# Kernel tuning notes

Measured on AMD Instinct MI355X. Metric: run time of the kernel, lower is better.

## Reference

```python
import math
import jax, jax.numpy as jnp
import numpy as np
from jax import lax

DN = ('NCHW', 'OIHW', 'NCHW')

def _blur(x):
    # upfirdn2d blur: separable [1,3,3,1] kernel, normalized, gain=factor^2=4, pad (1,1)
    k1 = jnp.asarray([1., 3., 3., 1.], dtype=x.dtype)
    k2 = jnp.outer(k1, k1)
    k2 = k2 / jnp.sum(k2) * 4.0
    C = x.shape[1]
    kern = jnp.broadcast_to(k2[None, None], (C, 1, 4, 4))
    return lax.conv_general_dilated(x, kern, (1, 1), [(1, 1), (1, 1)],
                                    feature_group_count=C, dimension_numbers=DN)

def _mod_conv(x, z, w, mw, mb, demodulate, upsample):
    # StyleGAN2 ModulatedConv2d. w: [Co,Ci,k,k]; mw: [Ci,style_dim]; mb: [Ci].
    # Equivalent formulation: scale input by style (per in-channel), conv with
    # base weight, rescale output by per-sample demod (per out-channel).
    Ci, k = w.shape[1], w.shape[-1]
    style = z @ mw.T * (1.0 / math.sqrt(mw.shape[1])) + mb  # EqualLinear -> [B, Ci]
    ws = w * (1.0 / math.sqrt(Ci * k * k))
    if demodulate:
        wmod = ws[None] * style[:, None, :, None, None]              # [B,Co,Ci,k,k]
        demod = lax.rsqrt(jnp.sum(wmod * wmod, axis=(2, 3, 4)) + 1e-8)  # [B,Co]
    x = x * style[:, :, None, None]
    if upsample:
        # torch conv_transpose2d(stride=2, pad=0) == direct conv with flipped kernel + lhs dilation
        kern = ws[:, :, ::-1, ::-1]
        x = lax.conv_general_dilated(x, kern, (1, 1), [(k - 1, k - 1)] * 2,
                                     lhs_dilation=(2, 2), dimension_numbers=DN)
    else:
        x = lax.conv_general_dilated(x, ws, (1, 1), [(k // 2, k // 2)] * 2,
                                     dimension_numbers=DN)
    if demodulate:
        x = x * demod[:, :, None, None]
    if upsample:
        x = _blur(x)
    return x

def _styled_conv(x, z, w, mw, mb, b, upsample):
    # StyledConv (use_noise=False): modulated conv + FusedLeakyReLU(bias, 0.2, gain sqrt(2))
    x = _mod_conv(x, z, w, mw, mb, True, upsample)
    return jax.nn.leaky_relu(x + b[None, :, None, None], 0.2) * math.sqrt(2.0)

def setup_inputs() -> dict:
    B, CIN, SD, S = 16, 256, 512, 32
    key = jax.random.key(0)
    ks = jax.random.split(key, 32)
    f32 = jnp.float32
    d = {
        'fg_feat': jax.random.normal(ks[0], (B, CIN, S, S), f32),
        'mask':    jax.random.uniform(ks[1], (B, S, S), f32),
        'bg_feat': jax.random.normal(ks[2], (B, CIN, S, S), f32),
        'z':       jax.random.normal(ks[3], (B, SD), f32),
    }
    # layer schedule: (cin, cout, upsample)
    layers = [(CIN, 128, False), (128, 128, True), (128, 64, False),
              (64, 64, True), (64, 32, False)]
    i = 4
    for li, (ci, co, _) in enumerate(layers):
        d[f'l{li}_w'] = jax.random.normal(ks[i], (co, ci, 3, 3), f32); i += 1
        d[f'l{li}_mw'] = jax.random.normal(ks[i], (ci, SD), f32); i += 1
        d[f'l{li}_mb'] = jnp.ones((ci,), f32)
        d[f'l{li}_b'] = jnp.zeros((co,), f32)
    d['fin_w'] = jax.random.normal(ks[i], (4, 32, 1, 1), f32); i += 1
    d['fin_mw'] = jax.random.normal(ks[i], (32, SD), f32); i += 1
    d['fin_mb'] = jnp.ones((32,), f32)
    d['out_bias'] = jnp.zeros((1, 4, 1, 1), f32)
    return d

def reference(fg_feat, mask, bg_feat, z,
              l0_w, l0_mw, l0_mb, l0_b,
              l1_w, l1_mw, l1_mb, l1_b,
              l2_w, l2_mw, l2_mb, l2_b,
              l3_w, l3_mw, l3_mb, l3_b,
              l4_w, l4_mw, l4_mb, l4_b,
              fin_w, fin_mw, fin_mb, out_bias):
    # bg_activation is None -> no bg transform
    h = fg_feat + (1.0 - mask[:, None]) * bg_feat          # [B,256,32,32]
    h = _styled_conv(h, z, l0_w, l0_mw, l0_mb, l0_b, False)  # [B,128,32,32]
    h = _styled_conv(h, z, l1_w, l1_mw, l1_mb, l1_b, True)   # [B,128,64,64]
    h = _styled_conv(h, z, l2_w, l2_mw, l2_mb, l2_b, False)  # [B,64,64,64]
    h = _styled_conv(h, z, l3_w, l3_mw, l3_mb, l3_b, True)   # [B,64,128,128]
    h = _styled_conv(h, z, l4_w, l4_mw, l4_mb, l4_b, False)  # [B,32,128,128]
    h = _mod_conv(h, z, fin_w, fin_mw, fin_mb, False, False) + out_bias  # [B,4,128,128]
    return h[:, :3]
```

## Files before the change

kernel.cpp:

```cpp
#include <hip/hip_runtime.h>
#include <math.h>

#define SQRT2 1.41421356237309515f

typedef __bf16 bf16x8 __attribute__((ext_vector_type(8)));
typedef float f32x4 __attribute__((ext_vector_type(4)));
typedef unsigned short u16x4 __attribute__((ext_vector_type(4)));
typedef unsigned short u16x8 __attribute__((ext_vector_type(8)));

__device__ __forceinline__ unsigned short f2bf(float f) {
    unsigned u = __builtin_bit_cast(unsigned, f);
    u += 0x7fffu + ((u >> 16) & 1u);
    return (unsigned short)(u >> 16);
}

__global__ __launch_bounds__(256) void style_all(
    const float* __restrict__ z,
    const float* __restrict__ mw0, const float* __restrict__ mb0,
    const float* __restrict__ mw1, const float* __restrict__ mb1,
    const float* __restrict__ mw2, const float* __restrict__ mb2,
    const float* __restrict__ mw3, const float* __restrict__ mb3,
    const float* __restrict__ mw4, const float* __restrict__ mb4,
    const float* __restrict__ mwf, const float* __restrict__ mbf,
    float* __restrict__ s0, float* __restrict__ s1, float* __restrict__ s2,
    float* __restrict__ s3, float* __restrict__ s4, float* __restrict__ sf) {
    int i = blockIdx.x * 256 + threadIdx.x;
    const float* mw; const float* mb; float* o; int Ci, idx; float mul = 1.f;
    if (i < 4096)       { mw = mw0; mb = mb0; o = s0; Ci = 256; idx = i; }
    else if (i < 6144)  { mw = mw1; mb = mb1; o = s1; Ci = 128; idx = i - 4096; }
    else if (i < 8192)  { mw = mw2; mb = mb2; o = s2; Ci = 128; idx = i - 6144; }
    else if (i < 9216)  { mw = mw3; mb = mb3; o = s3; Ci = 64;  idx = i - 8192; }
    else if (i < 10240) { mw = mw4; mb = mb4; o = s4; Ci = 64;  idx = i - 9216; }
    else if (i < 10752) { mw = mwf; mb = mbf; o = sf; Ci = 32;  idx = i - 10240;
                          mul = 0.1767766952966369f; }
    else return;
    int b = idx / Ci, ci = idx % Ci;
    const float* zp = z + b * 512;
    const float* wp = mw + ci * 512;
    float acc = 0.f;
#pragma unroll 8
    for (int k = 0; k < 512; ++k) acc += zp[k] * wp[k];
    o[idx] = (acc * 0.04419417382415922f + mb[ci]) * mul;
}

__global__ __launch_bounds__(256) void demod_all(
    const float* __restrict__ w0, const float* __restrict__ w1,
    const float* __restrict__ w2, const float* __restrict__ w3,
    const float* __restrict__ w4,
    const float* __restrict__ s0, const float* __restrict__ s1,
    const float* __restrict__ s2, const float* __restrict__ s3,
    const float* __restrict__ s4,
    float* __restrict__ d0, float* __restrict__ d1, float* __restrict__ d2,
    float* __restrict__ d3, float* __restrict__ d4) {
    int wid = blockIdx.x * 4 + (threadIdx.x >> 6);
    int lane = threadIdx.x & 63;
    const float* w; const float* s; float* d; int Co, Ci, idx;
    if (wid < 2048)      { w = w0; s = s0; d = d0; Co = 128; Ci = 256; idx = wid; }
    else if (wid < 4096) { w = w1; s = s1; d = d1; Co = 128; Ci = 128; idx = wid - 2048; }
    else if (wid < 5120) { w = w2; s = s2; d = d2; Co = 64;  Ci = 128; idx = wid - 4096; }
    else if (wid < 6144) { w = w3; s = s3; d = d3; Co = 64;  Ci = 64;  idx = wid - 5120; }
    else if (wid < 6656) { w = w4; s = s4; d = d4; Co = 32;  Ci = 64;  idx = wid - 6144; }
    else return;
    int b = idx / Co, co = idx % Co;
    const float* wp = w + (size_t)co * Ci * 9;
    const float* sp = s + b * Ci;
    float acc = 0.f;
    for (int k = lane; k < Ci * 9; k += 64) {
        int ci = k / 9;
        float v = wp[k], sv = sp[ci];
        acc += v * v * sv * sv;
    }
    for (int off = 32; off > 0; off >>= 1) acc += __shfl_down(acc, off);
    if (lane == 0) d[b * Co + co] = rsqrtf(acc / (float)(Ci * 9) + 1e-8f);
}

__device__ __forceinline__ void pack_cw_elem(
    const float* __restrict__ w, unsigned short* __restrict__ dst,
    int i, int Ci, int KT, float sInv) {
    int cil = i & 31;
    int r = i >> 5;
    int col = r % 32; r /= 32;
    int t = r % 9; r /= 9;
    int c = r % KT, g = r / KT;
    int co = g * 32 + col, ci = c * 32 + cil;
    dst[i] = f2bf(w[((size_t)co * Ci + ci) * 9 + t] * sInv);
}
__device__ __forceinline__ void pack_fused_elem(
    const float* __restrict__ w, unsigned short* __restrict__ dst,
    int i, int Ci, int KT, float sInv) {
    int cil = i & 31;
    int r = i >> 5;
    int col = r % 32; r /= 32;
    int t = r % 36; r /= 36;
    int c = r % KT, g = r / KT;
    int co = g * 32 + col, ci = c * 32 + cil;
    int p = t / 9, dd = (t % 9) / 3, ee = t % 3;
    int py = p >> 1, px = p & 1;
    const float k1[4] = {1.f, 3.f, 3.f, 1.f};
    const float* wq = w + ((size_t)co * Ci + ci) * 9;
    float acc = 0.f;
#pragma unroll
    for (int rr = 0; rr < 3; ++rr) {
        int ia = 2 * dd + rr - 1 - py;
        if (ia < 0 || ia > 3) continue;
#pragma unroll
        for (int ss = 0; ss < 3; ++ss) {
            int ib = 2 * ee + ss - 1 - px;
            if (ib < 0 || ib > 3) continue;
            acc += wq[rr * 3 + ss] * k1[ia] * k1[ib];
        }
    }
    dst[i] = f2bf(acc * sInv * (1.f / 16.f));
}

__global__ __launch_bounds__(256) void pack_all(
    const float* __restrict__ l0w, const float* __restrict__ l1w,
    const float* __restrict__ l2w, const float* __restrict__ l3w,
    const float* __restrict__ l4w, unsigned short* __restrict__ base) {
    const float sInv1152 = 0.02946278254943948f;
    int i = blockIdx.x * 256 + threadIdx.x;
    if (i < 294912)       pack_cw_elem(l0w, base, i, 256, 8, 1.f / 48.f);
    else if (i < 368640)  pack_cw_elem(l2w, base + 294912, i - 294912, 128, 4, sInv1152);
    else if (i < 387072)  pack_cw_elem(l4w, base + 368640, i - 368640, 64, 2, 1.f / 24.f);
    else if (i < 976896)  pack_fused_elem(l1w, base + 387072, i - 387072, 128, 4, sInv1152);
    else if (i < 1124352) pack_fused_elem(l3w, base + 976896, i - 976896, 64, 2, 1.f / 24.f);
}

__global__ __launch_bounds__(256) void composite_cl_kernel(
    const float* __restrict__ fg, const float* __restrict__ mask,
    const float* __restrict__ bg, const float* __restrict__ sty0,
    unsigned short* __restrict__ out) {
    __shared__ unsigned short ldsT[32 * 264];
    int blk = blockIdx.x;
    int b = blk >> 5, y = blk & 31;
    int t = threadIdx.x;
    int x = t & 31, cr = t >> 5;
    const float* sb = sty0 + b * 256;
    float m = 1.f - mask[(b << 10) + (y << 5) + x];
    for (int k = 0; k < 32; ++k) {
        int ci = k * 8 + cr;
        size_t idx = ((size_t)(b * 256 + ci) << 10) + (y << 5) + x;
        float v = fg[idx] + m * bg[idx];
        ldsT[x * 264 + ci] = f2bf(v * sb[ci]);
    }
    __syncthreads();
    int xx = t >> 5, cu = t & 31;
#pragma unroll
    for (int ph = 0; ph < 4; ++ph) {
        int px = ph * 8 + xx;
        u16x8 v = *(const u16x8*)&ldsT[px * 264 + cu * 8];
        *(u16x8*)(out + (((size_t)(b * 32 + y) * 32 + px) << 8) + cu * 8) = v;
    }
}

template <int OUTMODE>
__global__ __launch_bounds__(256, 4) void conv3x3_cl(
    const unsigned short* __restrict__ X, const unsigned short* __restrict__ W,
    const float* __restrict__ demod, const float* __restrict__ bias,
    const float* __restrict__ nextsty, const float* __restrict__ finw,
    const float* __restrict__ ob, void* __restrict__ outv,
    int Ci, int Co, int S, int TPS, int KCH, int cogN) {
    __shared__ unsigned short ldsX[324 * 40];
    const int tid = threadIdx.x;
    const int b = blockIdx.z;
    const int gy_ = blockIdx.y;
    const int ks = gy_ / cogN, cog = gy_ % cogN;
    const int tile = blockIdx.x;
    const int ty0 = (tile / TPS) * 16, tx0 = (tile % TPS) * 16;
    const int KT = Ci >> 5;
    const int wave = tid >> 6, lane = tid & 63, quad = lane >> 4, l16 = lane & 15;

    f32x4 acc[2][4];
#pragma unroll
    for (int mt = 0; mt < 2; ++mt)
#pragma unroll
        for (int nt = 0; nt < 4; ++nt) acc[mt][nt] = (f32x4){0.f, 0.f, 0.f, 0.f};

    for (int cc = 0; cc < KCH; ++cc) {
        const int cg = ks * KCH + cc;
        const int ci0 = cg * 32;
        for (int u = tid; u < 1296; u += 256) {
            int sp = u >> 2, cq = u & 3;
            int y = sp / 18, xx = sp - y * 18;
            int gy = ty0 - 1 + y, gx = tx0 - 1 + xx;
            u16x8 pk = (u16x8){0, 0, 0, 0, 0, 0, 0, 0};
            if ((unsigned)gy < (unsigned)S && (unsigned)gx < (unsigned)S)
                pk = *(const u16x8*)(X + ((size_t)(b * S + gy) * S + gx) * Ci + ci0 + cq * 8);
            *(u16x8*)&ldsX[sp * 40 + cq * 8] = pk;
        }
        __syncthreads();
        const unsigned short* wt = W + (((size_t)cog * KT + cg) * 9) * 1024;
#pragma unroll
        for (int t = 0; t < 9; ++t) {
            const int ty = t / 3, tx = t - ty * 3;
            bf16x8 af[2];
#pragma unroll
            for (int mt = 0; mt < 2; ++mt)
                af[mt] = *(const bf16x8*)(const void*)(wt + t * 1024 + (mt * 16 + l16) * 32 + quad * 8);
#pragma unroll
            for (int nt = 0; nt < 4; ++nt) {
                int sp = (wave * 4 + nt + ty) * 18 + l16 + tx;
                bf16x8 bv = *(const bf16x8*)(const void*)&ldsX[sp * 40 + quad * 8];
#pragma unroll
                for (int mt = 0; mt < 2; ++mt)
                    acc[mt][nt] = __builtin_amdgcn_mfma_f32_16x16x32_bf16(af[mt], bv, acc[mt][nt], 0, 0, 0);
            }
        }
        __syncthreads();
    }
    const int col = tx0 + l16;
    if (OUTMODE == 0) {
        float* out = (float*)outv;
        const size_t PS = (size_t)16 * S * S * Co;
#pragma unroll
        for (int mt = 0; mt < 2; ++mt) {
            int co0 = cog * 32 + mt * 16 + quad * 4;
#pragma unroll
            for (int nt = 0; nt < 4; ++nt) {
                int row = ty0 + wave * 4 + nt;
                *(f32x4*)&out[ks * PS + ((size_t)(b * S + row) * S + col) * Co + co0] = acc[mt][nt];
            }
        }
    } else if (OUTMODE == 1) {
#pragma unroll
        for (int mt = 0; mt < 2; ++mt) {
            int co0 = cog * 32 + mt * 16 + quad * 4;
            f32x4 dm = *(const f32x4*)&demod[b * Co + co0];
            f32x4 bi = *(const f32x4*)&bias[co0];
            f32x4 ns = *(const f32x4*)&nextsty[b * Co + co0];
#pragma unroll
            for (int nt = 0; nt < 4; ++nt) {
                int row = ty0 + wave * 4 + nt;
                size_t base = ((size_t)(b * S + row) * S + col) * Co + co0;
                u16x4 st;
#pragma unroll
                for (int r = 0; r < 4; ++r) {
                    float v = acc[mt][nt][r] * dm[r] + bi[r];
                    v = (v > 0.f ? v : 0.2f * v) * SQRT2 * ns[r];
                    st[r] = f2bf(v);
                }
                *(u16x4*)((unsigned short*)outv + base) = st;
            }
        }
    } else {
        f32x4 dm[2], bi[2], ns[2];
        float fw[3][2][4];
#pragma unroll
        for (int mt = 0; mt < 2; ++mt) {
            int c0 = mt * 16 + quad * 4;
            dm[mt] = *(const f32x4*)&demod[b * Co + c0];
            bi[mt] = *(const f32x4*)&bias[c0];
            ns[mt] = *(const f32x4*)&nextsty[b * Co + c0];
#pragma unroll
            for (int c = 0; c < 3; ++c)
#pragma unroll
                for (int r = 0; r < 4; ++r) fw[c][mt][r] = finw[c * 32 + c0 + r];
        }
        float* out = (float*)outv;
        float ob0 = ob[0], ob1 = ob[1], ob2 = ob[2];
#pragma unroll
        for (int nt = 0; nt < 4; ++nt) {
            int row = ty0 + wave * 4 + nt;
            float p0 = 0.f, p1 = 0.f, p2 = 0.f;
#pragma unroll
            for (int mt = 0; mt < 2; ++mt)
#pragma unroll
                for (int r = 0; r < 4; ++r) {
                    float v = acc[mt][nt][r] * dm[mt][r] + bi[mt][r];
                    v = (v > 0.f ? v : 0.2f * v) * SQRT2 * ns[mt][r];
                    p0 += v * fw[0][mt][r];
                    p1 += v * fw[1][mt][r];
                    p2 += v * fw[2][mt][r];
                }
            p0 += __shfl_xor(p0, 16); p0 += __shfl_xor(p0, 32);
            p1 += __shfl_xor(p1, 16); p1 += __shfl_xor(p1, 32);
            p2 += __shfl_xor(p2, 16); p2 += __shfl_xor(p2, 32);
            if (quad == 0) {
                size_t base = (((size_t)b * 3) << 14) + (row << 7) + col;
                out[base] = p0 + ob0;
                out[base + 16384] = p1 + ob1;
                out[base + 32768] = p2 + ob2;
            }
        }
    }
}

__global__ __launch_bounds__(256) void combine_l0_kernel(
    const float* __restrict__ P, const float* __restrict__ demod,
    const float* __restrict__ bias, const float* __restrict__ sty1,
    unsigned short* __restrict__ out) {
    int i = blockIdx.x * 256 + threadIdx.x;
    int co = i & 127;
    int b = i >> 17;
    float v = P[i] + P[i + (1 << 21)];
    v = v * demod[b * 128 + co] + bias[co];
    v = (v > 0.f ? v : 0.2f * v) * SQRT2 * sty1[b * 128 + co];
    out[i] = f2bf(v);
}

__global__ __launch_bounds__(256, 4) void upblur_cl(
    const unsigned short* __restrict__ X, const unsigned short* __restrict__ EW,
    const float* __restrict__ demod, const float* __restrict__ bias,
    const float* __restrict__ nextsty, unsigned short* __restrict__ out,
    int Ci, int Co, int S, int TPS) {
    __shared__ unsigned short ldsX[324 * 40];
    const int tid = threadIdx.x;
    const int b = blockIdx.z;
    const int cog = blockIdx.y >> 2, p = blockIdx.y & 3;
    const int tile = blockIdx.x;
    const int ty0 = (tile / TPS) * 16, tx0 = (tile % TPS) * 16;
    const int KT = Ci >> 5;
    const int wave = tid >> 6, lane = tid & 63, quad = lane >> 4, l16 = lane & 15;

    f32x4 acc[2][4];
#pragma unroll
    for (int mt = 0; mt < 2; ++mt)
#pragma unroll
        for (int nt = 0; nt < 4; ++nt) acc[mt][nt] = (f32x4){0.f, 0.f, 0.f, 0.f};

    for (int cc = 0; cc < KT; ++cc) {
        const int ci0 = cc * 32;
        for (int u = tid; u < 1296; u += 256) {
            int sp = u >> 2, cq = u & 3;
            int y = sp / 18, xx = sp - y * 18;
            int gy = ty0 - 1 + y, gx = tx0 - 1 + xx;
            u16x8 pk = (u16x8){0, 0, 0, 0, 0, 0, 0, 0};
            if ((unsigned)gy < (unsigned)S && (unsigned)gx < (unsigned)S)
                pk = *(const u16x8*)(X + ((size_t)(b * S + gy) * S + gx) * Ci + ci0 + cq * 8);
            *(u16x8*)&ldsX[sp * 40 + cq * 8] = pk;
        }
        __syncthreads();
        const unsigned short* wt = EW + (((size_t)cog * KT + cc) * 36 + p * 9) * 1024;
#pragma unroll
        for (int t = 0; t < 9; ++t) {
            const int dd = t / 3, ee = t - dd * 3;
            bf16x8 af[2];
#pragma unroll
            for (int mt = 0; mt < 2; ++mt)
                af[mt] = *(const bf16x8*)(const void*)(wt + t * 1024 + (mt * 16 + l16) * 32 + quad * 8);
#pragma unroll
            for (int nt = 0; nt < 4; ++nt) {
                int sp = (wave * 4 + nt + dd) * 18 + l16 + ee;
                bf16x8 bv = *(const bf16x8*)(const void*)&ldsX[sp * 40 + quad * 8];
#pragma unroll
                for (int mt = 0; mt < 2; ++mt)
                    acc[mt][nt] = __builtin_amdgcn_mfma_f32_16x16x32_bf16(af[mt], bv, acc[mt][nt], 0, 0, 0);
            }
        }
        __syncthreads();
    }
    const int S2 = 2 * S;
    const int py = p >> 1, px = p & 1;
    const int Xc = tx0 + l16, ox = 2 * Xc + px;
#pragma unroll
    for (int mt = 0; mt < 2; ++mt) {
        const int co0 = cog * 32 + mt * 16 + quad * 4;
        f32x4 dm = *(const f32x4*)&demod[b * Co + co0];
        f32x4 bi = *(const f32x4*)&bias[co0];
        f32x4 ns = *(const f32x4*)&nextsty[b * Co + co0];
#pragma unroll
        for (int nt = 0; nt < 4; ++nt) {
            int Y = ty0 + wave * 4 + nt, oy = 2 * Y + py;
            u16x4 st;
#pragma unroll
            for (int r = 0; r < 4; ++r) {
                float v = acc[mt][nt][r] * dm[r] + bi[r];
                v = (v > 0.f ? v : 0.2f * v) * SQRT2 * ns[r];
                st[r] = f2bf(v);
            }
            *(u16x4*)(out + ((size_t)(b * S2 + oy) * S2 + ox) * Co + co0) = st;
        }
    }
}

extern "C" void kernel_launch(void* const* d_in, const int* in_sizes, int n_in,
                              void* d_out, int out_size, void* d_ws, size_t ws_size,
                              hipStream_t stream) {
    const float* fg   = (const float*)d_in[0];
    const float* mask = (const float*)d_in[1];
    const float* bg   = (const float*)d_in[2];
    const float* z    = (const float*)d_in[3];
    const float* l0_w = (const float*)d_in[4];
    const float* l0_mw= (const float*)d_in[5];
    const float* l0_mb= (const float*)d_in[6];
    const float* l0_b = (const float*)d_in[7];
    const float* l1_w = (const float*)d_in[8];
    const float* l1_mw= (const float*)d_in[9];
    const float* l1_mb= (const float*)d_in[10];
    const float* l1_b = (const float*)d_in[11];
    const float* l2_w = (const float*)d_in[12];
    const float* l2_mw= (const float*)d_in[13];
    const float* l2_mb= (const float*)d_in[14];
    const float* l2_b = (const float*)d_in[15];
    const float* l3_w = (const float*)d_in[16];
    const float* l3_mw= (const float*)d_in[17];
    const float* l3_mb= (const float*)d_in[18];
    const float* l3_b = (const float*)d_in[19];
    const float* l4_w = (const float*)d_in[20];
    const float* l4_mw= (const float*)d_in[21];
    const float* l4_mb= (const float*)d_in[22];
    const float* l4_b = (const float*)d_in[23];
    const float* fin_w = (const float*)d_in[24];
    const float* fin_mw= (const float*)d_in[25];
    const float* fin_mb= (const float*)d_in[26];
    const float* obias = (const float*)d_in[27];

    float* wsf = (float*)d_ws;
    float* sty0 = wsf + 0;
    float* sty1 = wsf + 4096;
    float* sty2 = wsf + 6144;
    float* sty3 = wsf + 8192;
    float* sty4 = wsf + 9216;
    float* styf = wsf + 10240;
    float* dm0  = wsf + 10752;
    float* dm1  = wsf + 12800;
    float* dm2  = wsf + 14848;
    float* dm3  = wsf + 15872;
    float* dm4  = wsf + 16896;
    unsigned short* wbase = (unsigned short*)(wsf + 17408);
    unsigned short* wp0 = wbase;
    unsigned short* wp2 = wbase + 294912;
    unsigned short* wp4 = wbase + 368640;
    unsigned short* ew1 = wbase + 387072;
    unsigned short* ew3 = wbase + 976896;
    unsigned short* X0  = (unsigned short*)(wsf + 600000);
    float* Pbuf = wsf + 2697152;
    unsigned short* Y0  = (unsigned short*)(wsf + 6891456);
    unsigned short* Z1  = (unsigned short*)(wsf + 7940032);
    unsigned short* Y2  = X0;
    unsigned short* Z3  = (unsigned short*)(wsf + 12134336);

    dim3 blk(256);

    style_all<<<42, blk, 0, stream>>>(z, l0_mw, l0_mb, l1_mw, l1_mb, l2_mw, l2_mb,
                                      l3_mw, l3_mb, l4_mw, l4_mb, fin_mw, fin_mb,
                                      sty0, sty1, sty2, sty3, sty4, styf);
    demod_all<<<1664, blk, 0, stream>>>(l0_w, l1_w, l2_w, l3_w, l4_w,
                                        sty0, sty1, sty2, sty3, sty4,
                                        dm0, dm1, dm2, dm3, dm4);
    pack_all<<<4392, blk, 0, stream>>>(l0_w, l1_w, l2_w, l3_w, l4_w, wbase);

    composite_cl_kernel<<<512, blk, 0, stream>>>(fg, mask, bg, sty0, X0);

    conv3x3_cl<0><<<dim3(4, 8, 16), blk, 0, stream>>>(X0, wp0, nullptr, nullptr, nullptr, nullptr, nullptr, Pbuf, 256, 128, 32, 2, 4, 4);
    combine_l0_kernel<<<8192, blk, 0, stream>>>(Pbuf, dm0, l0_b, sty1, Y0);

    upblur_cl<<<dim3(4, 16, 16), blk, 0, stream>>>(Y0, ew1, dm1, l1_b, sty2, Z1, 128, 128, 32, 2);

    conv3x3_cl<1><<<dim3(16, 2, 16), blk, 0, stream>>>(Z1, wp2, dm2, l2_b, sty3, nullptr, nullptr, Y2, 128, 64, 64, 4, 4, 2);

    upblur_cl<<<dim3(16, 8, 16), blk, 0, stream>>>(Y2, ew3, dm3, l3_b, sty4, Z3, 64, 64, 64, 4);

    conv3x3_cl<3><<<dim3(64, 1, 16), blk, 0, stream>>>(Z3, wp4, dm4, l4_b, styf, fin_w, obias, (float*)d_out, 64, 32, 128, 8, 2, 1);
}
```

Measured before the change: 303.8 us.

## Drop LDS staging in 3x3 conv kernels; load input fragments directly from global

Both conv3x3_cl and upblur_cl stop staging an 18x18x32 input halo tile in shared memory behind barriers. Each lane now loads its own 6-row column of B fragments straight from global memory, once per horizontal tap, and reuses them across the three vertical taps. This removes the LDS writes and reads and both __syncthreads per channel chunk. In exchange, halo data is fetched redundantly by overlapping waves and lanes, global loads are no longer coalesced through a cooperative loop, and launch bounds drop to 3 blocks per CU to allow more registers.

```diff
diff --git a/kernel.cpp b/kernel.cpp
--- a/kernel.cpp
+++ b/kernel.cpp
@@ -154,17 +154,15 @@
 }
 
 template <int OUTMODE>
-__global__ __launch_bounds__(256, 4) void conv3x3_cl(
+__global__ __launch_bounds__(256, 3) void conv3x3_cl(
     const unsigned short* __restrict__ X, const unsigned short* __restrict__ W,
     const float* __restrict__ demod, const float* __restrict__ bias,
     const float* __restrict__ nextsty, const float* __restrict__ finw,
     const float* __restrict__ ob, void* __restrict__ outv,
     int Ci, int Co, int S, int TPS, int KCH, int cogN) {
-    __shared__ unsigned short ldsX[324 * 40];
     const int tid = threadIdx.x;
     const int b = blockIdx.z;
-    const int gy_ = blockIdx.y;
-    const int ks = gy_ / cogN, cog = gy_ % cogN;
+    const int ks = blockIdx.y / cogN, cog = blockIdx.y % cogN;
     const int tile = blockIdx.x;
     const int ty0 = (tile / TPS) * 16, tx0 = (tile % TPS) * 16;
     const int KT = Ci >> 5;
@@ -176,37 +174,38 @@
 #pragma unroll
         for (int nt = 0; nt < 4; ++nt) acc[mt][nt] = (f32x4){0.f, 0.f, 0.f, 0.f};
 
+    const int gyb = ty0 - 1 + wave * 4;
+    const int gxb = tx0 - 1 + l16;
+
     for (int cc = 0; cc < KCH; ++cc) {
         const int cg = ks * KCH + cc;
-        const int ci0 = cg * 32;
-        for (int u = tid; u < 1296; u += 256) {
-            int sp = u >> 2, cq = u & 3;
-            int y = sp / 18, xx = sp - y * 18;
-            int gy = ty0 - 1 + y, gx = tx0 - 1 + xx;
-            u16x8 pk = (u16x8){0, 0, 0, 0, 0, 0, 0, 0};
-            if ((unsigned)gy < (unsigned)S && (unsigned)gx < (unsigned)S)
-                pk = *(const u16x8*)(X + ((size_t)(b * S + gy) * S + gx) * Ci + ci0 + cq * 8);
-            *(u16x8*)&ldsX[sp * 40 + cq * 8] = pk;
-        }
-        __syncthreads();
-        const unsigned short* wt = W + (((size_t)cog * KT + cg) * 9) * 1024;
-#pragma unroll
-        for (int t = 0; t < 9; ++t) {
-            const int ty = t / 3, tx = t - ty * 3;
-            bf16x8 af[2];
-#pragma unroll
-            for (int mt = 0; mt < 2; ++mt)
-                af[mt] = *(const bf16x8*)(const void*)(wt + t * 1024 + (mt * 16 + l16) * 32 + quad * 8);
-#pragma unroll
-            for (int nt = 0; nt < 4; ++nt) {
-                int sp = (wave * 4 + nt + ty) * 18 + l16 + tx;
-                bf16x8 bv = *(const bf16x8*)(const void*)&ldsX[sp * 40 + quad * 8];
-#pragma unroll
-                for (int mt = 0; mt < 2; ++mt)
-                    acc[mt][nt] = __builtin_amdgcn_mfma_f32_16x16x32_bf16(af[mt], bv, acc[mt][nt], 0, 0, 0);
-            }
-        }
-        __syncthreads();
+        const unsigned short* xb = X + (size_t)cg * 32 + quad * 8;
+        const unsigned short* wt = W + (((size_t)cog * KT + cg) * 9) * 1024 + l16 * 32 + quad * 8;
+#pragma unroll
+        for (int ee = 0; ee < 3; ++ee) {
+            const int gx = gxb + ee;
+            const bool okx = (unsigned)gx < (unsigned)S;
+            bf16x8 bfr[6];
+#pragma unroll
+            for (int rr = 0; rr < 6; ++rr) {
+                int gy = gyb + rr;
+                u16x8 v = (u16x8){0, 0, 0, 0, 0, 0, 0, 0};
+                if (okx && (unsigned)gy < (unsigned)S)
+                    v = *(const u16x8*)(xb + ((size_t)(b * S + gy) * S + gx) * Ci);
+                bfr[rr] = __builtin_bit_cast(bf16x8, v);
+            }
+#pragma unroll
+            for (int ty = 0; ty < 3; ++ty) {
+                const int t = ty * 3 + ee;
+                bf16x8 af0 = *(const bf16x8*)(const void*)(wt + t * 1024);
+                bf16x8 af1 = *(const bf16x8*)(const void*)(wt + t * 1024 + 512);
+#pragma unroll
+                for (int nt = 0; nt < 4; ++nt) {
+                    acc[0][nt] = __builtin_amdgcn_mfma_f32_16x16x32_bf16(af0, bfr[nt + ty], acc[0][nt], 0, 0, 0);
+                    acc[1][nt] = __builtin_amdgcn_mfma_f32_16x16x32_bf16(af1, bfr[nt + ty], acc[1][nt], 0, 0, 0);
+                }
+            }
+        }
     }
     const int col = tx0 + l16;
     if (OUTMODE == 0) {
@@ -298,12 +297,11 @@
     out[i] = f2bf(v);
 }
 
-__global__ __launch_bounds__(256, 4) void upblur_cl(
+__global__ __launch_bounds__(256, 3) void upblur_cl(
     const unsigned short* __restrict__ X, const unsigned short* __restrict__ EW,
     const float* __restrict__ demod, const float* __restrict__ bias,
     const float* __restrict__ nextsty, unsigned short* __restrict__ out,
     int Ci, int Co, int S, int TPS) {
-    __shared__ unsigned short ldsX[324 * 40];
     const int tid = threadIdx.x;
     const int b = blockIdx.z;
     const int cog = blockIdx.y >> 2, p = blockIdx.y & 3;
@@ -318,36 +316,37 @@
 #pragma unroll
         for (int nt = 0; nt < 4; ++nt) acc[mt][nt] = (f32x4){0.f, 0.f, 0.f, 0.f};
 
+    const int gyb = ty0 - 1 + wave * 4;
+    const int gxb = tx0 - 1 + l16;
+
     for (int cc = 0; cc < KT; ++cc) {
-        const int ci0 = cc * 32;
-        for (int u = tid; u < 1296; u += 256) {
-            int sp = u >> 2, cq = u & 3;
-            int y = sp / 18, xx = sp - y * 18;
-            int gy = ty0 - 1 + y, gx = tx0 - 1 + xx;
-            u16x8 pk = (u16x8){0, 0, 0, 0, 0, 0, 0, 0};
-            if ((unsigned)gy < (unsigned)S && (unsigned)gx < (unsigned)S)
-                pk = *(const u16x8*)(X + ((size_t)(b * S + gy) * S + gx) * Ci + ci0 + cq * 8);
-            *(u16x8*)&ldsX[sp * 40 + cq * 8] = pk;
-        }
-        __syncthreads();
-        const unsigned short* wt = EW + (((size_t)cog * KT + cc) * 36 + p * 9) * 1024;
-#pragma unroll
-        for (int t = 0; t < 9; ++t) {
-            const int dd = t / 3, ee = t - dd * 3;
-            bf16x8 af[2];
-#pragma unroll
-            for (int mt = 0; mt < 2; ++mt)
-                af[mt] = *(const bf16x8*)(const void*)(wt + t * 1024 + (mt * 16 + l16) * 32 + quad * 8);
-#pragma unroll
-            for (int nt = 0; nt < 4; ++nt) {
-                int sp = (wave * 4 + nt + dd) * 18 + l16 + ee;
-                bf16x8 bv = *(const bf16x8*)(const void*)&ldsX[sp * 40 + quad * 8];
-#pragma unroll
-                for (int mt = 0; mt < 2; ++mt)
-                    acc[mt][nt] = __builtin_amdgcn_mfma_f32_16x16x32_bf16(af[mt], bv, acc[mt][nt], 0, 0, 0);
-            }
-        }
-        __syncthreads();
+        const unsigned short* xb = X + (size_t)cc * 32 + quad * 8;
+        const unsigned short* wt = EW + (((size_t)cog * KT + cc) * 36 + p * 9) * 1024 + l16 * 32 + quad * 8;
+#pragma unroll
+        for (int ee = 0; ee < 3; ++ee) {
+            const int gx = gxb + ee;
+            const bool okx = (unsigned)gx < (unsigned)S;
+            bf16x8 bfr[6];
+#pragma unroll
+            for (int rr = 0; rr < 6; ++rr) {
+                int gy = gyb + rr;
+                u16x8 v = (u16x8){0, 0, 0, 0, 0, 0, 0, 0};
+                if (okx && (unsigned)gy < (unsigned)S)
+                    v = *(const u16x8*)(xb + ((size_t)(b * S + gy) * S + gx) * Ci);
+                bfr[rr] = __builtin_bit_cast(bf16x8, v);
+            }
+#pragma unroll
+            for (int dd = 0; dd < 3; ++dd) {
+                const int t = dd * 3 + ee;
+                bf16x8 af0 = *(const bf16x8*)(const void*)(wt + t * 1024);
+                bf16x8 af1 = *(const bf16x8*)(const void*)(wt + t * 1024 + 512);
+#pragma unroll
+                for (int nt = 0; nt < 4; ++nt) {
+                    acc[0][nt] = __builtin_amdgcn_mfma_f32_16x16x32_bf16(af0, bfr[nt + dd], acc[0][nt], 0, 0, 0);
+                    acc[1][nt] = __builtin_amdgcn_mfma_f32_16x16x32_bf16(af1, bfr[nt + dd], acc[1][nt], 0, 0, 0);
+                }
+            }
+        }
     }
     const int S2 = 2 * S;
     const int py = p >> 1, px = p & 1;
```

After: 376.8 us. +24.0%, slower.

## Widen output-channel tile to 64 per block and shrink LDS row padding

Applied to the files above, without the earlier changes.

The conv and upblur kernels are templated on MT, so a block now computes 64 output channels (4 MFMA row tiles) instead of 32. Each LDS input tile is reused across twice as many MFMAs, and fewer blocks reload the same activations. Layer 0 now uses a 4-way split-K instead of 2-way, so the combine kernel sums four partials. Workspace buffers are moved to fit the larger partial buffer, and the LDS row stride is cut from 40 to 36 halfwords. The cost is higher register pressure (launch bounds lowered to 3 blocks per SM), fewer blocks in flight, and a possible change in LDS bank conflicts from the new stride.

```diff
diff --git a/kernel.cpp b/kernel.cpp
--- a/kernel.cpp
+++ b/kernel.cpp
@@ -76,24 +76,24 @@
 
 __device__ __forceinline__ void pack_cw_elem(
     const float* __restrict__ w, unsigned short* __restrict__ dst,
-    int i, int Ci, int KT, float sInv) {
+    int i, int Ci, int KT, int CoG, float sInv) {
     int cil = i & 31;
     int r = i >> 5;
-    int col = r % 32; r /= 32;
+    int col = r % CoG; r /= CoG;
     int t = r % 9; r /= 9;
     int c = r % KT, g = r / KT;
-    int co = g * 32 + col, ci = c * 32 + cil;
+    int co = g * CoG + col, ci = c * 32 + cil;
     dst[i] = f2bf(w[((size_t)co * Ci + ci) * 9 + t] * sInv);
 }
 __device__ __forceinline__ void pack_fused_elem(
     const float* __restrict__ w, unsigned short* __restrict__ dst,
-    int i, int Ci, int KT, float sInv) {
+    int i, int Ci, int KT, int CoG, float sInv) {
     int cil = i & 31;
     int r = i >> 5;
-    int col = r % 32; r /= 32;
+    int col = r % CoG; r /= CoG;
     int t = r % 36; r /= 36;
     int c = r % KT, g = r / KT;
-    int co = g * 32 + col, ci = c * 32 + cil;
+    int co = g * CoG + col, ci = c * 32 + cil;
     int p = t / 9, dd = (t % 9) / 3, ee = t % 3;
     int py = p >> 1, px = p & 1;
     const float k1[4] = {1.f, 3.f, 3.f, 1.f};
@@ -119,11 +119,11 @@
     const float* __restrict__ l4w, unsigned short* __restrict__ base) {
     const float sInv1152 = 0.02946278254943948f;
     int i = blockIdx.x * 256 + threadIdx.x;
-    if (i < 294912)       pack_cw_elem(l0w, base, i, 256, 8, 1.f / 48.f);
-    else if (i < 368640)  pack_cw_elem(l2w, base + 294912, i - 294912, 128, 4, sInv1152);
-    else if (i < 387072)  pack_cw_elem(l4w, base + 368640, i - 368640, 64, 2, 1.f / 24.f);
-    else if (i < 976896)  pack_fused_elem(l1w, base + 387072, i - 387072, 128, 4, sInv1152);
-    else if (i < 1124352) pack_fused_elem(l3w, base + 976896, i - 976896, 64, 2, 1.f / 24.f);
+    if (i < 294912)       pack_cw_elem(l0w, base, i, 256, 8, 64, 1.f / 48.f);
+    else if (i < 368640)  pack_cw_elem(l2w, base + 294912, i - 294912, 128, 4, 64, sInv1152);
+    else if (i < 387072)  pack_cw_elem(l4w, base + 368640, i - 368640, 64, 2, 32, 1.f / 24.f);
+    else if (i < 976896)  pack_fused_elem(l1w, base + 387072, i - 387072, 128, 4, 64, sInv1152);
+    else if (i < 1124352) pack_fused_elem(l3w, base + 976896, i - 976896, 64, 2, 64, 1.f / 24.f);
 }
 
 __global__ __launch_bounds__(256) void composite_cl_kernel(
@@ -153,26 +153,26 @@
     }
 }
 
-template <int OUTMODE>
-__global__ __launch_bounds__(256, 4) void conv3x3_cl(
+template <int MT, int OUTMODE>
+__global__ __launch_bounds__(256, 3) void conv3x3_cl(
     const unsigned short* __restrict__ X, const unsigned short* __restrict__ W,
     const float* __restrict__ demod, const float* __restrict__ bias,
     const float* __restrict__ nextsty, const float* __restrict__ finw,
     const float* __restrict__ ob, void* __restrict__ outv,
     int Ci, int Co, int S, int TPS, int KCH, int cogN) {
-    __shared__ unsigned short ldsX[324 * 40];
+    __shared__ unsigned short ldsX[324 * 36];
+    const int CoG = MT * 16;
     const int tid = threadIdx.x;
     const int b = blockIdx.z;
-    const int gy_ = blockIdx.y;
-    const int ks = gy_ / cogN, cog = gy_ % cogN;
+    const int ks = blockIdx.y / cogN, cog = blockIdx.y % cogN;
     const int tile = blockIdx.x;
     const int ty0 = (tile / TPS) * 16, tx0 = (tile % TPS) * 16;
     const int KT = Ci >> 5;
     const int wave = tid >> 6, lane = tid & 63, quad = lane >> 4, l16 = lane & 15;
 
-    f32x4 acc[2][4];
-#pragma unroll
-    for (int mt = 0; mt < 2; ++mt)
+    f32x4 acc[MT][4];
+#pragma unroll
+    for (int mt = 0; mt < MT; ++mt)
 #pragma unroll
         for (int nt = 0; nt < 4; ++nt) acc[mt][nt] = (f32x4){0.f, 0.f, 0.f, 0.f};
 
@@ -186,23 +186,23 @@
             u16x8 pk = (u16x8){0, 0, 0, 0, 0, 0, 0, 0};
             if ((unsigned)gy < (unsigned)S && (unsigned)gx < (unsigned)S)
                 pk = *(const u16x8*)(X + ((size_t)(b * S + gy) * S + gx) * Ci + ci0 + cq * 8);
-            *(u16x8*)&ldsX[sp * 40 + cq * 8] = pk;
+            *(u16x8*)&ldsX[sp * 36 + cq * 8] = pk;
         }
         __syncthreads();
-        const unsigned short* wt = W + (((size_t)cog * KT + cg) * 9) * 1024;
+        const unsigned short* wt = W + (((size_t)cog * KT + cg) * 9) * (CoG * 32) + l16 * 32 + quad * 8;
 #pragma unroll
         for (int t = 0; t < 9; ++t) {
             const int ty = t / 3, tx = t - ty * 3;
-            bf16x8 af[2];
-#pragma unroll
-            for (int mt = 0; mt < 2; ++mt)
-                af[mt] = *(const bf16x8*)(const void*)(wt + t * 1024 + (mt * 16 + l16) * 32 + quad * 8);
+            bf16x8 af[MT];
+#pragma unroll
+            for (int mt = 0; mt < MT; ++mt)
+                af[mt] = *(const bf16x8*)(const void*)(wt + t * (CoG * 32) + mt * 512);
 #pragma unroll
             for (int nt = 0; nt < 4; ++nt) {
                 int sp = (wave * 4 + nt + ty) * 18 + l16 + tx;
-                bf16x8 bv = *(const bf16x8*)(const void*)&ldsX[sp * 40 + quad * 8];
-#pragma unroll
-                for (int mt = 0; mt < 2; ++mt)
+                bf16x8 bv = *(const bf16x8*)(const void*)&ldsX[sp * 36 + quad * 8];
+#pragma unroll
+                for (int mt = 0; mt < MT; ++mt)
                     acc[mt][nt] = __builtin_amdgcn_mfma_f32_16x16x32_bf16(af[mt], bv, acc[mt][nt], 0, 0, 0);
             }
         }
@@ -213,8 +213,8 @@
         float* out = (float*)outv;
         const size_t PS = (size_t)16 * S * S * Co;
 #pragma unroll
-        for (int mt = 0; mt < 2; ++mt) {
-            int co0 = cog * 32 + mt * 16 + quad * 4;
+        for (int mt = 0; mt < MT; ++mt) {
+            int co0 = cog * CoG + mt * 16 + quad * 4;
 #pragma unroll
             for (int nt = 0; nt < 4; ++nt) {
                 int row = ty0 + wave * 4 + nt;
@@ -223,8 +223,8 @@
         }
     } else if (OUTMODE == 1) {
 #pragma unroll
-        for (int mt = 0; mt < 2; ++mt) {
-            int co0 = cog * 32 + mt * 16 + quad * 4;
+        for (int mt = 0; mt < MT; ++mt) {
+            int co0 = cog * CoG + mt * 16 + quad * 4;
             f32x4 dm = *(const f32x4*)&demod[b * Co + co0];
             f32x4 bi = *(const f32x4*)&bias[co0];
             f32x4 ns = *(const f32x4*)&nextsty[b * Co + co0];
@@ -243,10 +243,10 @@
             }
         }
     } else {
-        f32x4 dm[2], bi[2], ns[2];
-        float fw[3][2][4];
-#pragma unroll
-        for (int mt = 0; mt < 2; ++mt) {
+        f32x4 dm[MT], bi[MT], ns[MT];
+        float fw[3][MT][4];
+#pragma unroll
+        for (int mt = 0; mt < MT; ++mt) {
             int c0 = mt * 16 + quad * 4;
             dm[mt] = *(const f32x4*)&demod[b * Co + c0];
             bi[mt] = *(const f32x4*)&bias[c0];
@@ -263,7 +263,7 @@
             int row = ty0 + wave * 4 + nt;
             float p0 = 0.f, p1 = 0.f, p2 = 0.f;
 #pragma unroll
-            for (int mt = 0; mt < 2; ++mt)
+            for (int mt = 0; mt < MT; ++mt)
 #pragma unroll
                 for (int r = 0; r < 4; ++r) {
                     float v = acc[mt][nt][r] * dm[mt][r] + bi[mt][r];
@@ -290,20 +290,23 @@
     const float* __restrict__ bias, const float* __restrict__ sty1,
     unsigned short* __restrict__ out) {
     int i = blockIdx.x * 256 + threadIdx.x;
+    const int PS = 1 << 21;
     int co = i & 127;
     int b = i >> 17;
-    float v = P[i] + P[i + (1 << 21)];
+    float v = (P[i] + P[i + PS]) + (P[i + 2 * PS] + P[i + 3 * PS]);
     v = v * demod[b * 128 + co] + bias[co];
     v = (v > 0.f ? v : 0.2f * v) * SQRT2 * sty1[b * 128 + co];
     out[i] = f2bf(v);
 }
 
-__global__ __launch_bounds__(256, 4) void upblur_cl(
+template <int MT>
+__global__ __launch_bounds__(256, 3) void upblur_cl(
     const unsigned short* __restrict__ X, const unsigned short* __restrict__ EW,
     const float* __restrict__ demod, const float* __restrict__ bias,
     const float* __restrict__ nextsty, unsigned short* __restrict__ out,
     int Ci, int Co, int S, int TPS) {
-    __shared__ unsigned short ldsX[324 * 40];
+    __shared__ unsigned short ldsX[324 * 36];
+    const int CoG = MT * 16;
     const int tid = threadIdx.x;
     const int b = blockIdx.z;
     const int cog = blockIdx.y >> 2, p = blockIdx.y & 3;
@@ -312,9 +315,9 @@
     const int KT = Ci >> 5;
     const int wave = tid >> 6, lane = tid & 63, quad = lane >> 4, l16 = lane & 15;
 
-    f32x4 acc[2][4];
-#pragma unroll
-    for (int mt = 0; mt < 2; ++mt)
+    f32x4 acc[MT][4];
+#pragma unroll
+    for (int mt = 0; mt < MT; ++mt)
 #pragma unroll
         for (int nt = 0; nt < 4; ++nt) acc[mt][nt] = (f32x4){0.f, 0.f, 0.f, 0.f};
 
@@ -327,23 +330,23 @@
             u16x8 pk = (u16x8){0, 0, 0, 0, 0, 0, 0, 0};
             if ((unsigned)gy < (unsigned)S && (unsigned)gx < (unsigned)S)
                 pk = *(const u16x8*)(X + ((size_t)(b * S + gy) * S + gx) * Ci + ci0 + cq * 8);
-            *(u16x8*)&ldsX[sp * 40 + cq * 8] = pk;
+            *(u16x8*)&ldsX[sp * 36 + cq * 8] = pk;
         }
         __syncthreads();
-        const unsigned short* wt = EW + (((size_t)cog * KT + cc) * 36 + p * 9) * 1024;
+        const unsigned short* wt = EW + (((size_t)cog * KT + cc) * 36 + p * 9) * (CoG * 32) + l16 * 32 + quad * 8;
 #pragma unroll
         for (int t = 0; t < 9; ++t) {
             const int dd = t / 3, ee = t - dd * 3;
-            bf16x8 af[2];
-#pragma unroll
-            for (int mt = 0; mt < 2; ++mt)
-                af[mt] = *(const bf16x8*)(const void*)(wt + t * 1024 + (mt * 16 + l16) * 32 + quad * 8);
+            bf16x8 af[MT];
+#pragma unroll
+            for (int mt = 0; mt < MT; ++mt)
+                af[mt] = *(const bf16x8*)(const void*)(wt + t * (CoG * 32) + mt * 512);
 #pragma unroll
             for (int nt = 0; nt < 4; ++nt) {
                 int sp = (wave * 4 + nt + dd) * 18 + l16 + ee;
-                bf16x8 bv = *(const bf16x8*)(const void*)&ldsX[sp * 40 + quad * 8];
-#pragma unroll
-                for (int mt = 0; mt < 2; ++mt)
+                bf16x8 bv = *(const bf16x8*)(const void*)&ldsX[sp * 36 + quad * 8];
+#pragma unroll
+                for (int mt = 0; mt < MT; ++mt)
                     acc[mt][nt] = __builtin_amdgcn_mfma_f32_16x16x32_bf16(af[mt], bv, acc[mt][nt], 0, 0, 0);
             }
         }
@@ -353,8 +356,8 @@
     const int py = p >> 1, px = p & 1;
     const int Xc = tx0 + l16, ox = 2 * Xc + px;
 #pragma unroll
-    for (int mt = 0; mt < 2; ++mt) {
-        const int co0 = cog * 32 + mt * 16 + quad * 4;
+    for (int mt = 0; mt < MT; ++mt) {
+        const int co0 = cog * CoG + mt * 16 + quad * 4;
         f32x4 dm = *(const f32x4*)&demod[b * Co + co0];
         f32x4 bi = *(const f32x4*)&bias[co0];
         f32x4 ns = *(const f32x4*)&nextsty[b * Co + co0];
@@ -425,10 +428,10 @@
     unsigned short* ew3 = wbase + 976896;
     unsigned short* X0  = (unsigned short*)(wsf + 600000);
     float* Pbuf = wsf + 2697152;
-    unsigned short* Y0  = (unsigned short*)(wsf + 6891456);
-    unsigned short* Z1  = (unsigned short*)(wsf + 7940032);
+    unsigned short* Y0  = (unsigned short*)(wsf + 11085760);
+    unsigned short* Z1  = (unsigned short*)(wsf + 12134336);
     unsigned short* Y2  = X0;
-    unsigned short* Z3  = (unsigned short*)(wsf + 12134336);
+    unsigned short* Z3  = (unsigned short*)(wsf + 16328640);
 
     dim3 blk(256);
 
@@ -442,14 +445,14 @@
 
     composite_cl_kernel<<<512, blk, 0, stream>>>(fg, mask, bg, sty0, X0);
 
-    conv3x3_cl<0><<<dim3(4, 8, 16), blk, 0, stream>>>(X0, wp0, nullptr, nullptr, nullptr, nullptr, nullptr, Pbuf, 256, 128, 32, 2, 4, 4);
+    conv3x3_cl<4, 0><<<dim3(4, 8, 16), blk, 0, stream>>>(X0, wp0, nullptr, nullptr, nullptr, nullptr, nullptr, Pbuf, 256, 128, 32, 2, 2, 2);
     combine_l0_kernel<<<8192, blk, 0, stream>>>(Pbuf, dm0, l0_b, sty1, Y0);
 
-    upblur_cl<<<dim3(4, 16, 16), blk, 0, stream>>>(Y0, ew1, dm1, l1_b, sty2, Z1, 128, 128, 32, 2);
-
-    conv3x3_cl<1><<<dim3(16, 2, 16), blk, 0, stream>>>(Z1, wp2, dm2, l2_b, sty3, nullptr, nullptr, Y2, 128, 64, 64, 4, 4, 2);
-
-    upblur_cl<<<dim3(16, 8, 16), blk, 0, stream>>>(Y2, ew3, dm3, l3_b, sty4, Z3, 64, 64, 64, 4);
-
-    conv3x3_cl<3><<<dim3(64, 1, 16), blk, 0, stream>>>(Z3, wp4, dm4, l4_b, styf, fin_w, obias, (float*)d_out, 64, 32, 128, 8, 2, 1);
-}
+    upblur_cl<4><<<dim3(4, 8, 16), blk, 0, stream>>>(Y0, ew1, dm1, l1_b, sty2, Z1, 128, 128, 32, 2);
+
+    conv3x3_cl<4, 1><<<dim3(16, 1, 16), blk, 0, stream>>>(Z1, wp2, dm2, l2_b, sty3, nullptr, nullptr, Y2, 128, 64, 64, 4, 4, 1);
+
+    upblur_cl<4><<<dim3(16, 4, 16), blk, 0, stream>>>(Y2, ew3, dm3, l3_b, sty4, Z3, 64, 64, 64, 4);
+
+    conv3x3_cl<2, 3><<<dim3(64, 1, 16), blk, 0, stream>>>(Z3, wp4, dm4, l4_b, styf, fin_w, obias, (float*)d_out, 64, 32, 128, 8, 2, 1);
+}
```

After: 322.0 us. 1.06x slower.

## Give each wave a private LDS halo slab and drop block barriers

Applied to the files above, without the earlier changes.

The conv and upsample kernels now have each wave stage its own 6x18 input halo into a private LDS slab, so the __syncthreads barriers around the staged tile go away. The cost is redundant halo loads, since neighbouring waves overlap by two rows, which raises global and LDS traffic by about 1.5x. The row stride drops from 40 to 36 halfwords, which may change LDS bank conflicts. Layer 0 also splits K four ways instead of two to launch more blocks, which needs a four-way partial-sum combine and relocated workspace buffers.

```diff
diff --git a/kernel.cpp b/kernel.cpp
--- a/kernel.cpp
+++ b/kernel.cpp
@@ -160,53 +160,49 @@
     const float* __restrict__ nextsty, const float* __restrict__ finw,
     const float* __restrict__ ob, void* __restrict__ outv,
     int Ci, int Co, int S, int TPS, int KCH, int cogN) {
-    __shared__ unsigned short ldsX[324 * 40];
+    __shared__ unsigned short ldsX[4 * 3888];
     const int tid = threadIdx.x;
     const int b = blockIdx.z;
-    const int gy_ = blockIdx.y;
-    const int ks = gy_ / cogN, cog = gy_ % cogN;
+    const int ks = blockIdx.y / cogN, cog = blockIdx.y % cogN;
     const int tile = blockIdx.x;
     const int ty0 = (tile / TPS) * 16, tx0 = (tile % TPS) * 16;
     const int KT = Ci >> 5;
     const int wave = tid >> 6, lane = tid & 63, quad = lane >> 4, l16 = lane & 15;
+    unsigned short* slab = &ldsX[wave * 3888];
 
     f32x4 acc[2][4];
 #pragma unroll
     for (int mt = 0; mt < 2; ++mt)
 #pragma unroll
         for (int nt = 0; nt < 4; ++nt) acc[mt][nt] = (f32x4){0.f, 0.f, 0.f, 0.f};
+
+    const int gy0 = ty0 + wave * 4 - 1;
 
     for (int cc = 0; cc < KCH; ++cc) {
         const int cg = ks * KCH + cc;
         const int ci0 = cg * 32;
-        for (int u = tid; u < 1296; u += 256) {
-            int sp = u >> 2, cq = u & 3;
-            int y = sp / 18, xx = sp - y * 18;
-            int gy = ty0 - 1 + y, gx = tx0 - 1 + xx;
+        for (int u = lane; u < 432; u += 64) {
+            int cq = u & 3, sp = u >> 2;
+            int row = sp / 18, col = sp - row * 18;
+            int gy = gy0 + row, gx = tx0 - 1 + col;
             u16x8 pk = (u16x8){0, 0, 0, 0, 0, 0, 0, 0};
             if ((unsigned)gy < (unsigned)S && (unsigned)gx < (unsigned)S)
                 pk = *(const u16x8*)(X + ((size_t)(b * S + gy) * S + gx) * Ci + ci0 + cq * 8);
-            *(u16x8*)&ldsX[sp * 40 + cq * 8] = pk;
-        }
-        __syncthreads();
-        const unsigned short* wt = W + (((size_t)cog * KT + cg) * 9) * 1024;
+            *(u16x8*)&slab[sp * 36 + cq * 8] = pk;
+        }
+        const unsigned short* wt = W + (((size_t)cog * KT + cg) * 9) * 1024 + l16 * 32 + quad * 8;
 #pragma unroll
         for (int t = 0; t < 9; ++t) {
             const int ty = t / 3, tx = t - ty * 3;
-            bf16x8 af[2];
-#pragma unroll
-            for (int mt = 0; mt < 2; ++mt)
-                af[mt] = *(const bf16x8*)(const void*)(wt + t * 1024 + (mt * 16 + l16) * 32 + quad * 8);
+            bf16x8 af0 = *(const bf16x8*)(const void*)(wt + t * 1024);
+            bf16x8 af1 = *(const bf16x8*)(const void*)(wt + t * 1024 + 512);
 #pragma unroll
             for (int nt = 0; nt < 4; ++nt) {
-                int sp = (wave * 4 + nt + ty) * 18 + l16 + tx;
-                bf16x8 bv = *(const bf16x8*)(const void*)&ldsX[sp * 40 + quad * 8];
-#pragma unroll
-                for (int mt = 0; mt < 2; ++mt)
-                    acc[mt][nt] = __builtin_amdgcn_mfma_f32_16x16x32_bf16(af[mt], bv, acc[mt][nt], 0, 0, 0);
-            }
-        }
-        __syncthreads();
+                bf16x8 bv = *(const bf16x8*)(const void*)&slab[((nt + ty) * 18 + l16 + tx) * 36 + quad * 8];
+                acc[0][nt] = __builtin_amdgcn_mfma_f32_16x16x32_bf16(af0, bv, acc[0][nt], 0, 0, 0);
+                acc[1][nt] = __builtin_amdgcn_mfma_f32_16x16x32_bf16(af1, bv, acc[1][nt], 0, 0, 0);
+            }
+        }
     }
     const int col = tx0 + l16;
     if (OUTMODE == 0) {
@@ -290,9 +286,10 @@
     const float* __restrict__ bias, const float* __restrict__ sty1,
     unsigned short* __restrict__ out) {
     int i = blockIdx.x * 256 + threadIdx.x;
+    const int PS = 1 << 21;
     int co = i & 127;
     int b = i >> 17;
-    float v = P[i] + P[i + (1 << 21)];
+    float v = (P[i] + P[i + PS]) + (P[i + 2 * PS] + P[i + 3 * PS]);
     v = v * demod[b * 128 + co] + bias[co];
     v = (v > 0.f ? v : 0.2f * v) * SQRT2 * sty1[b * 128 + co];
     out[i] = f2bf(v);
@@ -303,7 +300,7 @@
     const float* __restrict__ demod, const float* __restrict__ bias,
     const float* __restrict__ nextsty, unsigned short* __restrict__ out,
     int Ci, int Co, int S, int TPS) {
-    __shared__ unsigned short ldsX[324 * 40];
+    __shared__ unsigned short ldsX[4 * 3888];
     const int tid = threadIdx.x;
     const int b = blockIdx.z;
     const int cog = blockIdx.y >> 2, p = blockIdx.y & 3;
@@ -311,43 +308,40 @@
     const int ty0 = (tile / TPS) * 16, tx0 = (tile % TPS) * 16;
     const int KT = Ci >> 5;
     const int wave = tid >> 6, lane = tid & 63, quad = lane >> 4, l16 = lane & 15;
+    unsigned short* slab = &ldsX[wave * 3888];
 
     f32x4 acc[2][4];
 #pragma unroll
     for (int mt = 0; mt < 2; ++mt)
 #pragma unroll
         for (int nt = 0; nt < 4; ++nt) acc[mt][nt] = (f32x4){0.f, 0.f, 0.f, 0.f};
+
+    const int gy0 = ty0 + wave * 4 - 1;
 
     for (int cc = 0; cc < KT; ++cc) {
         const int ci0 = cc * 32;
-        for (int u = tid; u < 1296; u += 256) {
-            int sp = u >> 2, cq = u & 3;
-            int y = sp / 18, xx = sp - y * 18;
-            int gy = ty0 - 1 + y, gx = tx0 - 1 + xx;
+        for (int u = lane; u < 432; u += 64) {
+            int cq = u & 3, sp = u >> 2;
+            int row = sp / 18, col = sp - row * 18;
+            int gy = gy0 + row, gx = tx0 - 1 + col;
             u16x8 pk = (u16x8){0, 0, 0, 0, 0, 0, 0, 0};
             if ((unsigned)gy < (unsigned)S && (unsigned)gx < (unsigned)S)
                 pk = *(const u16x8*)(X + ((size_t)(b * S + gy) * S + gx) * Ci + ci0 + cq * 8);
-            *(u16x8*)&ldsX[sp * 40 + cq * 8] = pk;
-        }
-        __syncthreads();
-        const unsigned short* wt = EW + (((size_t)cog * KT + cc) * 36 + p * 9) * 1024;
+            *(u16x8*)&slab[sp * 36 + cq * 8] = pk;
+        }
+        const unsigned short* wt = EW + (((size_t)cog * KT + cc) * 36 + p * 9) * 1024 + l16 * 32 + quad * 8;
 #pragma unroll
         for (int t = 0; t < 9; ++t) {
             const int dd = t / 3, ee = t - dd * 3;
-            bf16x8 af[2];
-#pragma unroll
-            for (int mt = 0; mt < 2; ++mt)
-                af[mt] = *(const bf16x8*)(const void*)(wt + t * 1024 + (mt * 16 + l16) * 32 + quad * 8);
+            bf16x8 af0 = *(const bf16x8*)(const void*)(wt + t * 1024);
+            bf16x8 af1 = *(const bf16x8*)(const void*)(wt + t * 1024 + 512);
 #pragma unroll
             for (int nt = 0; nt < 4; ++nt) {
-                int sp = (wave * 4 + nt + dd) * 18 + l16 + ee;
-                bf16x8 bv = *(const bf16x8*)(const void*)&ldsX[sp * 40 + quad * 8];
-#pragma unroll
-                for (int mt = 0; mt < 2; ++mt)
-                    acc[mt][nt] = __builtin_amdgcn_mfma_f32_16x16x32_bf16(af[mt], bv, acc[mt][nt], 0, 0, 0);
-            }
-        }
-        __syncthreads();
+                bf16x8 bv = *(const bf16x8*)(const void*)&slab[((nt + dd) * 18 + l16 + ee) * 36 + quad * 8];
+                acc[0][nt] = __builtin_amdgcn_mfma_f32_16x16x32_bf16(af0, bv, acc[0][nt], 0, 0, 0);
+                acc[1][nt] = __builtin_amdgcn_mfma_f32_16x16x32_bf16(af1, bv, acc[1][nt], 0, 0, 0);
+            }
+        }
     }
     const int S2 = 2 * S;
     const int py = p >> 1, px = p & 1;
@@ -425,10 +419,10 @@
     unsigned short* ew3 = wbase + 976896;
     unsigned short* X0  = (unsigned short*)(wsf + 600000);
     float* Pbuf = wsf + 2697152;
-    unsigned short* Y0  = (unsigned short*)(wsf + 6891456);
-    unsigned short* Z1  = (unsigned short*)(wsf + 7940032);
+    unsigned short* Y0  = (unsigned short*)(wsf + 11085760);
+    unsigned short* Z1  = (unsigned short*)(wsf + 12134336);
     unsigned short* Y2  = X0;
-    unsigned short* Z3  = (unsigned short*)(wsf + 12134336);
+    unsigned short* Z3  = (unsigned short*)(wsf + 16328640);
 
     dim3 blk(256);
 
@@ -442,7 +436,7 @@
 
     composite_cl_kernel<<<512, blk, 0, stream>>>(fg, mask, bg, sty0, X0);
 
-    conv3x3_cl<0><<<dim3(4, 8, 16), blk, 0, stream>>>(X0, wp0, nullptr, nullptr, nullptr, nullptr, nullptr, Pbuf, 256, 128, 32, 2, 4, 4);
+    conv3x3_cl<0><<<dim3(4, 16, 16), blk, 0, stream>>>(X0, wp0, nullptr, nullptr, nullptr, nullptr, nullptr, Pbuf, 256, 128, 32, 2, 2, 4);
     combine_l0_kernel<<<8192, blk, 0, stream>>>(Pbuf, dm0, l0_b, sty1, Y0);
 
     upblur_cl<<<dim3(4, 16, 16), blk, 0, stream>>>(Y0, ew1, dm1, l1_b, sty2, Z1, 128, 128, 32, 2);
```

New measurement: 360.2 us. +18.6%, slower.
